# Kernel optimization log

Measured on AMD Instinct MI355X. Metric: run time of the kernel, lower is better.

The kernel has to match this reference:

```python
import jax, jax.numpy as jnp
import numpy as np

B, K, V = 8192, 1024, 2


def setup_inputs() -> dict:
    key = jax.random.key(0)
    k1, k2, k3, k4, k5, k6 = jax.random.split(key, 6)
    z = jax.random.normal(k1, (B, K), dtype=jnp.float32)
    # -1 means no intervention for that sample
    intervention_target = jax.random.randint(k2, (B,), -1, K)
    intervention_variant = jax.random.randint(k3, (B,), 0, V)
    raw_adjacency = jax.random.normal(k4, (K, K), dtype=jnp.float32) * 0.05
    intervention_means = jax.random.normal(k5, (K, V), dtype=jnp.float32)
    intervention_log_scales = jax.random.normal(k6, (K, V), dtype=jnp.float32) * 0.1
    return {
        "z": z,
        "intervention_target": intervention_target,
        "intervention_variant": intervention_variant,
        "raw_adjacency": raw_adjacency,
        "intervention_means": intervention_means,
        "intervention_log_scales": intervention_log_scales,
    }


def _scm_forward(z, target, variant, raw_adjacency, means, log_scales):
    Kd = z.shape[1]
    # strictly-lower-triangular adjacency (row j holds parents of node j)
    A = raw_adjacency * jnp.tril(jnp.ones((Kd, Kd), z.dtype), k=-1)

    def step(u, xs):
        a_row, mean_row, logsc_row, z_j, j = xs
        # forward substitution: u_j = z_j + sum_{i<j} A[j,i] * u_i
        # columns >= j of u are still zero and A row is zero there too
        value = z_j + u @ a_row  # [B]
        # intervention overwrite for samples with target == j
        m = mean_row[variant]                 # [B]
        s = jnp.exp(logsc_row[variant])       # [B]
        value = jnp.where(target == j, m + s * z_j, value)
        u = jax.lax.dynamic_update_slice(u, value[:, None], (0, j))
        return u, None

    u0 = jnp.zeros_like(z)
    xs = (A, means, log_scales, z.T, jnp.arange(Kd))
    u, _ = jax.lax.scan(step, u0, xs)
    return u


def reference(z, intervention_target, intervention_variant, raw_adjacency,
              intervention_means, intervention_log_scales):
    return _scm_forward(z, intervention_target, intervention_variant,
                        raw_adjacency, intervention_means, intervention_log_scales)
```

## Files before the change

### kernel.cpp

```cpp
#include <hip/hip_runtime.h>
#include <hip/hip_bf16.h>
#include <cstdint>

#define KDIM 1024
#define BDIM 8192
#define VDIM 2
#define NBLK 16

#if defined(__has_builtin)
#if __has_builtin(__builtin_amdgcn_global_load_lds)
#define HAS_GLL 1
#endif
#endif
#ifndef HAS_GLL
#define HAS_GLL 0
#endif

typedef __attribute__((ext_vector_type(8))) short short8;
typedef __attribute__((ext_vector_type(4))) float f32x4;

__device__ inline unsigned short f2bf(float x) {
  unsigned u = __builtin_bit_cast(unsigned, x);
  u = (u + 0x7FFFu + ((u >> 16) & 1u)) >> 16;
  return (unsigned short)u;
}

__device__ inline float bf2f(unsigned short x) {
  return __builtin_bit_cast(float, (unsigned)x << 16);
}


#define STAGE_T(DST, SRC, ROW0, COL0, LD)                                   \
  {                                                                         \
    const float* _s = (SRC);                                                \
    _Pragma("unroll") for (int _p = 0; _p < 4; ++_p) {                      \
      const int _m = _p * 16 + rw;                                          \
      float4 _v = *(const float4*)(_s + (size_t)((ROW0) + _m) * (LD) +      \
                                   (COL0) + 4 * k4);                        \
      (DST)[4 * k4 + 0][_m] = _v.x;                                         \
      (DST)[4 * k4 + 1][_m] = _v.y;                                         \
      (DST)[4 * k4 + 2][_m] = _v.z;                                         \
      (DST)[4 * k4 + 3][_m] = _v.w;                                         \
    }                                                                       \
  }

#define STAGE_D(DST, SRC, ROW0, COL0, LD)                                   \
  {                                                                         \
    const float* _s = (SRC);                                                \
    _Pragma("unroll") for (int _p = 0; _p < 4; ++_p) {                      \
      const int _kk = _p * 16 + rw;                                         \
      *(float4*)&(DST)[_kk][4 * k4] =                                       \
          *(const float4*)(_s + (size_t)((ROW0) + _kk) * (LD) + (COL0) +    \
                           4 * k4);                                         \
    }                                                                       \
  }

#define LOADR(REG, SRC, ROW0, COL0, LD)                                     \
  _Pragma("unroll") for (int _p = 0; _p < 4; ++_p) {                        \
    (REG)[_p] = *(const float4*)((SRC) +                                    \
                                 (size_t)((ROW0) + _p * 16 + rw) * (LD) +   \
                                 (COL0) + 4 * k4);                          \
  }

#define WRT_T(DST, REG)                                                     \
  _Pragma("unroll") for (int _p = 0; _p < 4; ++_p) {                        \
    const int _m = _p * 16 + rw;                                            \
    (DST)[4 * k4 + 0][_m] = (REG)[_p].x;                                    \
    (DST)[4 * k4 + 1][_m] = (REG)[_p].y;                                    \
    (DST)[4 * k4 + 2][_m] = (REG)[_p].z;                                    \
    (DST)[4 * k4 + 3][_m] = (REG)[_p].w;                                    \
  }

#define WRT_D(DST, REG)                                                     \
  _Pragma("unroll") for (int _p = 0; _p < 4; ++_p) {                        \
    *(float4*)&(DST)[_p * 16 + rw][4 * k4] = (REG)[_p];                     \
  }

#define ZERO_ACC                                                            \
  _Pragma("unroll") for (int _a = 0; _a < 4; ++_a)                          \
      _Pragma("unroll") for (int _b = 0; _b < 4; ++_b) acc[_a][_b] = 0.f;

__device__ __forceinline__ void mac64(const float (*Ls)[68],
                                      const float (*Rs)[68], int tm, int tn,
                                      float acc[4][4]) {
#pragma unroll 4
  for (int k = 0; k < 64; ++k) {
    const float4 av = *(const float4*)&Ls[k][4 * tm];
    const float4 bv = *(const float4*)&Rs[k][4 * tn];
    const float aa[4] = {av.x, av.y, av.z, av.w};
    const float bb4[4] = {bv.x, bv.y, bv.z, bv.w};
#pragma unroll
    for (int a = 0; a < 4; ++a)
#pragma unroll
      for (int b = 0; b < 4; ++b) acc[a][b] += aa[a] * bb4[b];
  }
}

#define STORE_MT(R0, C0)                                                    \
  _Pragma("unroll") for (int _a = 0; _a < 4; ++_a) {                        \
    *(float4*)(MT + (size_t)((R0) + 4 * tm + _a) * KDIM + (C0) + 4 * tn) =  \
        make_float4(acc[_a][0], acc[_a][1], acc[_a][2], acc[_a][3]);        \
  }

#define MBF_TILE(R0, C0, BUF)                                               \
  {                                                                         \
    __syncthreads();                                                        \
    _Pragma("unroll") for (int _a = 0; _a < 4; ++_a)                        \
        _Pragma("unroll") for (int _b = 0; _b < 4; ++_b)                    \
            (BUF)[4 * tm + _a][4 * tn + _b] = acc[_a][_b];                  \
    __syncthreads();                                                        \
    const int _tr = tid >> 4, _tc = tid & 15;                               \
    _Pragma("unroll") for (int _p = 0; _p < 4; ++_p) {                      \
      const int _il = _p * 16 + _tr;                                        \
      ushort4 _o;                                                           \
      _o.x = f2bf((BUF)[4 * _tc + 0][_il]);                                 \
      _o.y = f2bf((BUF)[4 * _tc + 1][_il]);                                 \
      _o.z = f2bf((BUF)[4 * _tc + 2][_il]);                                 \
      _o.w = f2bf((BUF)[4 * _tc + 3][_il]);                                 \
      *(ushort4*)(Mbf + (size_t)((C0) + _il) * KDIM + (R0) + 4 * _tc) = _o; \
    }                                                                       \
  }

__global__ __launch_bounds__(256) void comb01(const float* __restrict__ A,
                                              float* __restrict__ MT,
                                              unsigned short* __restrict__ Mbf,
                                              const float* __restrict__ Z,
                                              unsigned short* __restrict__ Zbf,
                                              int do_zbf) {
  if (blockIdx.x >= NBLK) {
    const int wid = blockIdx.x - NBLK;
    const int nw = gridDim.x - NBLK;
    const int idx0 = wid * 256 + threadIdx.x;
    const int stride = nw * 256;
    const float4 z4 = make_float4(0.f, 0.f, 0.f, 0.f);
    const uint4 u4 = make_uint4(0u, 0u, 0u, 0u);

    for (int i = idx0; i < 256 * 1024; i += stride) {
      const int blk = i >> 10, off = i & 1023;
      const int bi = blk >> 4, bj = blk & 15;
      if (bi <= bj) continue;
      *(float4*)(MT + (size_t)(bi * 64 + (off >> 4)) * KDIM + bj * 64 +
                 4 * (off & 15)) = z4;
    }
    for (int i = idx0; i < 256 * 512; i += stride) {
      const int blk = i >> 9, off = i & 511;
      const int bi = blk >> 4, bj = blk & 15;
      if (bi >= bj) continue;
      *(uint4*)(Mbf + (size_t)(bi * 64 + (off >> 3)) * KDIM + bj * 64 +
                8 * (off & 7)) = u4;
    }
    if (do_zbf) {
      for (int i = idx0; i < BDIM * KDIM / 4; i += stride) {
        float4 v = *(const float4*)(Z + 4 * (size_t)i);
        ushort4 o;
        o.x = f2bf(v.x);
        o.y = f2bf(v.y);
        o.z = f2bf(v.z);
        o.w = f2bf(v.w);
        *(ushort4*)(Zbf + 4 * (size_t)i) = o;
      }
    }
    return;
  }

  int b = blockIdx.x;
  const int rt = b & 1;
  const int jt = (b >> 1) & 1;
  const int s = b >> 2;
  const int base = s * 256;

  __shared__ float shpool[6 * 64 * 68];
  float (*Ls)[68] = (float(*)[68])(shpool);
  float (*Rs)[68] = (float(*)[68])(shpool + 4352);
  float (*tQ0L)[68] = (float(*)[68])(shpool + 2 * 4352);
  float (*tQ0H)[68] = (float(*)[68])(shpool + 3 * 4352);
  float (*tP0)[68] = (float(*)[68])(shpool + 4 * 4352);
  float (*tP1)[68] = (float(*)[68])(shpool + 5 * 4352);

  const int tid = threadIdx.x;
  const int k4 = tid & 15;
  const int rw = tid >> 4;
  const int tm = tid >> 4;
  const int tn = tid & 15;
  float acc[4][4];

  {
    float* Tt = shpool;
    float* As4 = shpool + 2 * 4352;
    const int g = tid >> 6;
    const int l = tid & 63;
    const int dbase = base + g * 64;
    float* Asg = As4 + g * 4160;

    for (int r = 0; r < 64; ++r)
      Asg[r * 65 + l] = A[(size_t)(dbase + r) * KDIM + dbase + l];
    __syncthreads();

    {
      const int h = l >> 5, c = l & 31;
      const float* Ah = Asg + (32 * h) * 65 + 32 * h;
      float m[32];
#pragma unroll
      for (int r = 0; r < 32; ++r) m[r] = (r == c) ? 1.f : 0.f;
#pragma unroll
      for (int r = 1; r < 32; ++r) {
        float a0 = 0.f, a1 = 0.f;
#pragma unroll
        for (int i = 0; i < 32; ++i) {
          if (i >= r) break;
          if (i & 1) a1 += Ah[r * 65 + i] * m[i];
          else       a0 += Ah[r * 65 + i] * m[i];
        }
        const float v = a0 + a1;
        m[r] = (r > c) ? v : m[r];
      }
      float* Th = Tt + g * 2112 + h * 1056;
#pragma unroll
      for (int r = 0; r < 32; ++r) Th[r * 33 + c] = m[r];
    }
    __syncthreads();

    const int tm8 = l >> 3, tn8 = l & 7;
    {
      float u[4][4];
#pragma unroll
      for (int a = 0; a < 4; ++a)
#pragma unroll
        for (int b2 = 0; b2 < 4; ++b2) u[a][b2] = 0.f;
      const float* T1 = Tt + g * 2112;
#pragma unroll
      for (int ki = 0; ki < 8; ++ki) {
        float4 av[4], bv[4];
#pragma unroll
        for (int a = 0; a < 4; ++a)
          av[a] = *(const float4*)&Asg[(32 + 4 * tm8 + a) * 65 + 4 * ki];
#pragma unroll
        for (int j = 0; j < 4; ++j)
          bv[j] = *(const float4*)&T1[(4 * ki + j) * 33 + 4 * tn8];
#pragma unroll
        for (int a = 0; a < 4; ++a) {
          const float aa[4] = {av[a].x, av[a].y, av[a].z, av[a].w};
#pragma unroll
          for (int j = 0; j < 4; ++j) {
            const float bb[4] = {bv[j].x, bv[j].y, bv[j].z, bv[j].w};
#pragma unroll
            for (int b2 = 0; b2 < 4; ++b2) u[a][b2] += aa[j] * bb[b2];
          }
        }
      }
#pragma unroll
      for (int a = 0; a < 4; ++a)
#pragma unroll
        for (int b2 = 0; b2 < 4; ++b2)
          Asg[(4 * tm8 + a) * 32 + 4 * tn8 + b2] = u[a][b2];
    }
    __syncthreads();

    {
      float t21[4][4];
#pragma unroll
      for (int a = 0; a < 4; ++a)
#pragma unroll
        for (int b2 = 0; b2 < 4; ++b2) t21[a][b2] = 0.f;
      const float* T2 = Tt + g * 2112 + 1056;
#pragma unroll
      for (int ki = 0; ki < 8; ++ki) {
        float4 av[4], bv[4];
#pragma unroll
        for (int a = 0; a < 4; ++a)
          av[a] = *(const float4*)&T2[(4 * tm8 + a) * 33 + 4 * ki];
#pragma unroll
        for (int j = 0; j < 4; ++j)
          bv[j] = *(const float4*)&Asg[(4 * ki + j) * 32 + 4 * tn8];
#pragma unroll
        for (int a = 0; a < 4; ++a) {
          const float aa[4] = {av[a].x, av[a].y, av[a].z, av[a].w};
#pragma unroll
          for (int j = 0; j < 4; ++j) {
            const float bb[4] = {bv[j].x, bv[j].y, bv[j].z, bv[j].w};
#pragma unroll
            for (int b2 = 0; b2 < 4; ++b2) t21[a][b2] += aa[j] * bb[b2];
          }
        }
      }
#pragma unroll
      for (int a = 0; a < 4; ++a)
#pragma unroll
        for (int b2 = 0; b2 < 4; ++b2)
          Asg[1024 + (4 * tm8 + a) * 32 + 4 * tn8 + b2] = t21[a][b2];
    }
    __syncthreads();

    {
      const float* T21 = Asg + 1024;
      const float* Tg = Tt + g * 2112;
      for (int r4 = 0; r4 < 16; ++r4) {
        float vals[4];
#pragma unroll
        for (int j = 0; j < 4; ++j) {
          const int r = 4 * r4 + j;
          float v;
          if (r < 32)
            v = (l < 32) ? Tg[r * 33 + l] : 0.f;
          else
            v = (l < 32) ? T21[(r - 32) * 32 + l]
                         : Tg[1056 + (r - 32) * 33 + (l - 32)];
          vals[j] = v;
        }
        *(float4*)(MT + (size_t)(dbase + l) * KDIM + dbase + 4 * r4) =
            make_float4(vals[0], vals[1], vals[2], vals[3]);
      }
      if (jt == 0 && rt == 0) {
        for (int r = 0; r < 64; ++r) {
          float v;
          if (r < 32)
            v = (l < 32) ? Tg[r * 33 + l] : 0.f;
          else
            v = (l < 32) ? T21[(r - 32) * 32 + l]
                         : Tg[1056 + (r - 32) * 33 + (l - 32)];
          Mbf[(size_t)(dbase + r) * KDIM + dbase + l] = f2bf(v);
        }
      }
    }
    __syncthreads();
  }

  if (jt == 0) {
    STAGE_T(Ls, MT, base, base, KDIM);
    STAGE_T(Rs, A, base + 64, base, KDIM);
    __syncthreads();
    ZERO_ACC;
    mac64(Ls, Rs, tm, tn, acc);
    __syncthreads();
#pragma unroll
    for (int a = 0; a < 4; ++a)
#pragma unroll
      for (int b2 = 0; b2 < 4; ++b2) tP0[4 * tn + b2][4 * tm + a] = acc[a][b2];
    STAGE_D(Rs, MT, base + 64, base + 64, KDIM);
    __syncthreads();
    ZERO_ACC;
    mac64(tP0, Rs, tm, tn, acc);
    __syncthreads();
#pragma unroll
    for (int a = 0; a < 4; ++a)
#pragma unroll
      for (int b2 = 0; b2 < 4; ++b2) tQ0L[4 * tn + b2][4 * tm + a] = acc[a][b2];
    if (rt == 0) {
      STORE_MT(base, base + 64);
      MBF_TILE(base, base + 64, Rs);
    }
  }
  __syncthreads();

  if (rt == 1) {
    STAGE_T(Ls, MT, base + 128, base + 128, KDIM);
    STAGE_T(Rs, A, base + 192, base + 128, KDIM);
    __syncthreads();
    ZERO_ACC;
    mac64(Ls, Rs, tm, tn, acc);
    __syncthreads();
#pragma unroll
    for (int a = 0; a < 4; ++a)
#pragma unroll
      for (int b2 = 0; b2 < 4; ++b2) tP1[4 * tn + b2][4 * tm + a] = acc[a][b2];
    STAGE_D(Rs, MT, base + 192, base + 192, KDIM);
    __syncthreads();
    ZERO_ACC;
    mac64(tP1, Rs, tm, tn, acc);
    __syncthreads();
#pragma unroll
    for (int a = 0; a < 4; ++a)
#pragma unroll
      for (int b2 = 0; b2 < 4; ++b2) tQ0H[4 * tm + a][4 * tn + b2] = acc[a][b2];
    if (jt == 1) {
      STORE_MT(base + 128, base + 192);
      MBF_TILE(base + 128, base + 192, Rs);
    }
  }
  __syncthreads();

  STAGE_T(Ls, MT, base + 64 * jt, base + 64 * jt, KDIM);
  __syncthreads();
  for (int kb2 = 0; kb2 <= rt; ++kb2) {
    ZERO_ACC;
    for (int kb = jt; kb < 2; ++kb) {
      STAGE_T(Rs, A, base + 128 + 64 * kb2, base + 64 * kb, KDIM);
      __syncthreads();
      mac64(kb == jt ? Ls : tQ0L, Rs, tm, tn, acc);
      __syncthreads();
    }
    if (kb2 == 0) {
#pragma unroll
      for (int a = 0; a < 4; ++a)
#pragma unroll
        for (int b2 = 0; b2 < 4; ++b2) tP0[4 * tn + b2][4 * tm + a] = acc[a][b2];
    } else {
#pragma unroll
      for (int a = 0; a < 4; ++a)
#pragma unroll
        for (int b2 = 0; b2 < 4; ++b2) tP1[4 * tn + b2][4 * tm + a] = acc[a][b2];
    }
  }
  __syncthreads();

  ZERO_ACC;
  if (rt == 0) {
    STAGE_D(Rs, MT, base + 128, base + 128, KDIM);
    __syncthreads();
    mac64(tP0, Rs, tm, tn, acc);
    __syncthreads();
  } else {
    mac64(tP0, tQ0H, tm, tn, acc);
    __syncthreads();
    STAGE_D(Rs, MT, base + 192, base + 192, KDIM);
    __syncthreads();
    mac64(tP1, Rs, tm, tn, acc);
    __syncthreads();
  }
  STORE_MT(base + 64 * jt, base + 128 + 64 * rt);
  MBF_TILE(base + 64 * jt, base + 128 + 64 * rt, Rs);
}

template <int T>
__global__ __launch_bounds__(256) void p_k(const float* __restrict__ A,
                                           const float* __restrict__ MT,
                                           float* __restrict__ Pt) {
  int b = blockIdx.x;
  const int rb = b % T; b /= T;
  const int jb = b % T; b /= T;
  const int c = b;
  const int h = 64 * T;
  const int base = c * 2 * h;

  __shared__ float Ls[64][68];
  __shared__ float Rs[64][68];
  const int tid = threadIdx.x;
  const int k4 = tid & 15;
  const int rw = tid >> 4;
  const int tm = tid >> 4;
  const int tn = tid & 15;
  float acc[4][4];
  ZERO_ACC;

  float4 lr[4], rr[4];
  LOADR(lr, MT, base + 64 * jb, base + 64 * jb, KDIM);
  LOADR(rr, A, base + h + 64 * rb, base + 64 * jb, KDIM);
  for (int kb = jb; kb < T; ++kb) {
    WRT_T(Ls, lr);
    WRT_T(Rs, rr);
    __syncthreads();
    if (kb + 1 < T) {
      LOADR(lr, MT, base + 64 * jb, base + 64 * (kb + 1), KDIM);
      LOADR(rr, A, base + h + 64 * rb, base + 64 * (kb + 1), KDIM);
    }
    mac64(Ls, Rs, tm, tn, acc);
    __syncthreads();
  }

  float* P0 = Pt + (size_t)c * h * h;
#pragma unroll
  for (int a = 0; a < 4; ++a)
    *(float4*)(P0 + (size_t)(64 * jb + 4 * tm + a) * h + 64 * rb + 4 * tn) =
        make_float4(acc[a][0], acc[a][1], acc[a][2], acc[a][3]);
}

template <int T>
__global__ __launch_bounds__(256) void q_k(float* __restrict__ MT,
                                           const float* __restrict__ Pt,
                                           unsigned short* __restrict__ Mbf) {
  int b = blockIdx.x;
  const int rb = b % T; b /= T;
  const int jb = b % T; b /= T;
  const int c = b;
  const int h = 64 * T;
  const int base = c * 2 * h;

  __shared__ float Ls[64][68];
  __shared__ float Rs[64][68];
  const int tid = threadIdx.x;
  const int k4 = tid & 15;
  const int rw = tid >> 4;
  const int tm = tid >> 4;
  const int tn = tid & 15;
  float acc[4][4];
  ZERO_ACC;

  const float* P0 = Pt + (size_t)c * h * h;
  float4 lr[4], rr[4];
  LOADR(lr, P0, 64 * jb, 0, h);
  LOADR(rr, MT, base + h, base + h + 64 * rb, KDIM);
  for (int kb = 0; kb <= rb; ++kb) {
    WRT_T(Ls, lr);
    WRT_D(Rs, rr);
    __syncthreads();
    if (kb + 1 <= rb) {
      LOADR(lr, P0, 64 * jb, 64 * (kb + 1), h);
      LOADR(rr, MT, base + h + 64 * (kb + 1), base + h + 64 * rb, KDIM);
    }
    mac64(Ls, Rs, tm, tn, acc);
    __syncthreads();
  }

  STORE_MT(base + 64 * jb, base + h + 64 * rb);
  MBF_TILE(base + 64 * jb, base + h + 64 * rb, Ls);
}

#define LDB 72

template <int ZBF>
__global__ __launch_bounds__(256) void gemm_mfma(
    const float* __restrict__ Z, const unsigned short* __restrict__ Zbf,
    const unsigned short* __restrict__ Mbf, const float* __restrict__ MT,
    const int* __restrict__ tgt, const int* __restrict__ var,
    const float* __restrict__ means, const float* __restrict__ lsc,
    float* __restrict__ C) {
  __shared__ unsigned short As[128][LDB];
#if HAS_GLL
  __shared__ unsigned short Bs[128][64];
#else
  __shared__ unsigned short Bs[128][LDB];
#endif
  __shared__ float scoef[128];
  __shared__ int stb[128];

  const int d = blockIdx.x;
  const int xbl = d & 7;
  const int nir = (d >> 3) & 7;
  const int xbh = d >> 6;
  const int xb = xbh * 8 + xbl;
  const int ni = (xb & 32) ? (7 - nir) : nir;
  const int b0 = xb * 128;
  const int i0 = ni * 128;

  const int tid = threadIdx.x;
  const int w = tid >> 6;
  const int lane = tid & 63;
  const int wr = w >> 1, wc = w & 1;
  const int mlane = lane & 15;
  const int q = lane >> 4;

  const int rq = tid >> 4, kq = tid & 15;
  const int cb = tid >> 3, ck = tid & 7;

  f32x4 acc[4][4];
#pragma unroll
  for (int a = 0; a < 4; ++a)
#pragma unroll
    for (int b = 0; b < 4; ++b) acc[a][b] = (f32x4){0.f, 0.f, 0.f, 0.f};

  const int nkb = 2 * (ni + 1);
  for (int kb = 0; kb < nkb; ++kb) {
    const int k0 = kb * 64;
    if (ZBF) {
#pragma unroll
      for (int p = 0; p < 4; ++p) {
        const int r = p * 32 + cb;
        *(uint4*)&As[r][8 * ck] =
            *(const uint4*)(Zbf + (size_t)(b0 + r) * KDIM + k0 + 8 * ck);
      }
    } else {
#pragma unroll
      for (int p = 0; p < 8; ++p) {
        const int r = p * 16 + rq;
        float4 zv = *(const float4*)(Z + (size_t)(b0 + r) * KDIM + k0 + 4 * kq);
        ushort4 o;
        o.x = f2bf(zv.x);
        o.y = f2bf(zv.y);
        o.z = f2bf(zv.z);
        o.w = f2bf(zv.w);
        *(ushort4*)&As[r][4 * kq] = o;
      }
    }
#if HAS_GLL
    {
      const int rl = lane >> 3;
      const int ch = lane & 7;
#pragma unroll
      for (int i = 0; i < 4; ++i) {
        const int row = w * 32 + i * 8 + rl;
        const int sch = ch ^ (row & 7);
        const unsigned short* src =
            Mbf + (size_t)(i0 + row) * KDIM + k0 + sch * 8;
        __builtin_amdgcn_global_load_lds(
            (const __attribute__((address_space(1))) void*)src,
            (__attribute__((address_space(3))) void*)&Bs[w * 32 + i * 8][0],
            16, 0, 0);
      }
    }
#else
#pragma unroll
    for (int p = 0; p < 4; ++p) {
      const int c = p * 32 + cb;
      *(uint4*)&Bs[c][8 * ck] =
          *(const uint4*)(Mbf + (size_t)(i0 + c) * KDIM + k0 + 8 * ck);
    }
#endif
    __syncthreads();
#pragma unroll
    for (int ks = 0; ks < 2; ++ks) {
      const int kf = ks * 32 + q * 8;
      short8 av[4], bv[4];
#pragma unroll
      for (int a = 0; a < 4; ++a)
        av[a] = *(const short8*)&As[wr * 64 + 16 * a + mlane][kf];
#if HAS_GLL
      const char* BsB = (const char*)&Bs[0][0];
#pragma unroll
      for (int b = 0; b < 4; ++b) {
        const int row = wc * 64 + 16 * b + mlane;
        bv[b] = *(const short8*)(BsB + row * 128 +
                                 ((2 * kf) ^ ((row & 7) << 4)));
      }
#else
#pragma unroll
      for (int b = 0; b < 4; ++b)
        bv[b] = *(const short8*)&Bs[wc * 64 + 16 * b + mlane][kf];
#endif
#pragma unroll
      for (int a = 0; a < 4; ++a)
#pragma unroll
        for (int b = 0; b < 4; ++b)
          acc[a][b] =
              __builtin_amdgcn_mfma_f32_16x16x32_bf16(av[a], bv[b], acc[a][b], 0, 0, 0);
    }
    __syncthreads();
  }

  {
    const int s = tid >> 1, h2 = tid & 1;
    const int br = b0 + s;
    const int tb = tgt[br];
    float part = 0.f;
    if (tb >= 0) {
      const int nk16 = (tb >> 4) + 1;
      if (ZBF) {
        const unsigned short* zr = Zbf + (size_t)br * KDIM;
        const unsigned short* mr = Mbf + (size_t)tb * KDIM;
        for (int c16 = h2; c16 < nk16; c16 += 2) {
          const uint4 za = *(const uint4*)(zr + c16 * 16);
          const uint4 zb2 = *(const uint4*)(zr + c16 * 16 + 8);
          const uint4 ma = *(const uint4*)(mr + c16 * 16);
          const uint4 mb2 = *(const uint4*)(mr + c16 * 16 + 8);
          const unsigned zw[8] = {za.x, za.y, za.z, za.w,
                                  zb2.x, zb2.y, zb2.z, zb2.w};
          const unsigned mw[8] = {ma.x, ma.y, ma.z, ma.w,
                                  mb2.x, mb2.y, mb2.z, mb2.w};
#pragma unroll
          for (int wv = 0; wv < 8; ++wv) {
            part += __builtin_bit_cast(float, zw[wv] << 16) *
                    __builtin_bit_cast(float, mw[wv] << 16);
            part += __builtin_bit_cast(float, zw[wv] & 0xFFFF0000u) *
                    __builtin_bit_cast(float, mw[wv] & 0xFFFF0000u);
          }
        }
      } else {
        const float* zr = Z + (size_t)br * KDIM;
        const unsigned short* mr = Mbf + (size_t)tb * KDIM;
        const int nk8 = (tb >> 3) + 1;
        for (int c8 = h2; c8 < nk8; c8 += 2) {
          const float4 z0 = *(const float4*)(zr + c8 * 8);
          const float4 z1 = *(const float4*)(zr + c8 * 8 + 4);
          const ushort4 m0 = *(const ushort4*)(mr + c8 * 8);
          const ushort4 m1 = *(const ushort4*)(mr + c8 * 8 + 4);
          part += z0.x * bf2f(m0.x) + z0.y * bf2f(m0.y) + z0.z * bf2f(m0.z) +
                  z0.w * bf2f(m0.w) + z1.x * bf2f(m1.x) + z1.y * bf2f(m1.y) +
                  z1.z * bf2f(m1.z) + z1.w * bf2f(m1.w);
        }
      }
    }
    part += __shfl_down(part, 1);
    if (h2 == 0) {
      float cf = 0.f;
      int tbs = 0;
      if (tb >= 0) {
        const int v = var[br];
        const float mval = means[tb * VDIM + v];
        const float sval = expf(lsc[tb * VDIM + v]);
        const float zv = Z[(size_t)br * KDIM + tb];
        cf = (mval + sval * zv) - part;
        tbs = tb;
      }
      scoef[s] = cf;
      stb[s] = tbs;
    }
  }
  __syncthreads();

#pragma unroll
  for (int a = 0; a < 4; ++a) {
    const int l0 = wr * 64 + 16 * a + q * 4;
    const int row0 = b0 + l0;
#pragma unroll
    for (int b = 0; b < 4; ++b) {
      const int col = i0 + wc * 64 + 16 * b + mlane;
      float* Cp = C + (size_t)row0 * KDIM + col;
#pragma unroll
      for (int j = 0; j < 4; ++j) {
        const float cf = scoef[l0 + j];
        const float corr = cf * MT[(size_t)stb[l0 + j] * KDIM + col];
        Cp[j * KDIM] = acc[a][b][j] + corr;
      }
    }
  }
}

extern "C" void kernel_launch(void* const* d_in, const int* in_sizes, int n_in,
                              void* d_out, int out_size, void* d_ws,
                              size_t ws_size, hipStream_t stream) {
  const float* z = (const float*)d_in[0];
  const int* tgt = (const int*)d_in[1];
  const int* var = (const int*)d_in[2];
  const float* A = (const float*)d_in[3];
  const float* means = (const float*)d_in[4];
  const float* lsc = (const float*)d_in[5];
  float* out = (float*)d_out;

  char* ws = (char*)d_ws;
  float* MT = (float*)ws;
  unsigned short* Mbf = (unsigned short*)(ws + (4u << 20));
  float* Pt2 = (float*)(ws + (6u << 20));
  float* Pt3 = (float*)(ws + (6u << 20) + (512u << 10));
  unsigned short* Zbf = (unsigned short*)(ws + (7u << 20) + (512u << 10));
  const int use_zbf =
      ws_size >= (7u << 20) + (512u << 10) + (size_t)BDIM * KDIM * 2 ? 1 : 0;

  hipLaunchKernelGGL(comb01, dim3(256), dim3(256), 0, stream, A, MT, Mbf, z,
                     Zbf, use_zbf);
  hipLaunchKernelGGL((p_k<4>), dim3(32), dim3(256), 0, stream, A, MT, Pt2);
  hipLaunchKernelGGL((q_k<4>), dim3(32), dim3(256), 0, stream, MT, Pt2, Mbf);
  hipLaunchKernelGGL((p_k<8>), dim3(64), dim3(256), 0, stream, A, MT, Pt3);
  hipLaunchKernelGGL((q_k<8>), dim3(64), dim3(256), 0, stream, MT, Pt3, Mbf);
  if (use_zbf)
    hipLaunchKernelGGL((gemm_mfma<1>), dim3((BDIM / 128) * (KDIM / 128)),
                       dim3(256), 0, stream, z, Zbf, Mbf, MT, tgt, var, means,
                       lsc, out);
  else
    hipLaunchKernelGGL((gemm_mfma<0>), dim3((BDIM / 128) * (KDIM / 128)),
                       dim3(256), 0, stream, z, Zbf, Mbf, MT, tgt, var, means,
                       lsc, out);
}
```

Baseline: 248.5 us.

## Split-K the triangular inverse combine steps with atomics for more parallelism

The P and Q combine kernels that build the inverse of (I - A) block by block used to loop serially over the inner 64-blocks inside each of only 32 or 64 workgroups. They are now split along the inner dimension, so each workgroup handles a single 64-block product and accumulates into P and MT with float atomics. Workgroups with no work in the triangular structure exit early. comb01 now pre-zeros the target MT tiles and the P scratch, and a new kernel converts those 96 tiles to bf16 afterwards. The aim is more parallelism on this latency-bound chain, at the cost of atomic traffic, an extra launch and an order of float summation that can vary between runs.

```diff
diff --git a/kernel.cpp b/kernel.cpp
--- a/kernel.cpp
+++ b/kernel.cpp
@@ -27,6 +27,19 @@
 
 __device__ inline float bf2f(unsigned short x) {
   return __builtin_bit_cast(float, (unsigned)x << 16);
+}
+
+__device__ inline void qtile_map(int t, int& bi, int& bj) {
+  if (t < 64) {
+    bi = t >> 3;
+    bj = 8 + (t & 7);
+  } else {
+    int r = t - 64;
+    const int c = r >> 4;
+    r &= 15;
+    bi = 8 * c + (r >> 2);
+    bj = 8 * c + 4 + (r & 3);
+  }
 }
 
 
@@ -53,27 +66,6 @@
           *(const float4*)(_s + (size_t)((ROW0) + _kk) * (LD) + (COL0) +    \
                            4 * k4);                                         \
     }                                                                       \
-  }
-
-#define LOADR(REG, SRC, ROW0, COL0, LD)                                     \
-  _Pragma("unroll") for (int _p = 0; _p < 4; ++_p) {                        \
-    (REG)[_p] = *(const float4*)((SRC) +                                    \
-                                 (size_t)((ROW0) + _p * 16 + rw) * (LD) +   \
-                                 (COL0) + 4 * k4);                          \
-  }
-
-#define WRT_T(DST, REG)                                                     \
-  _Pragma("unroll") for (int _p = 0; _p < 4; ++_p) {                        \
-    const int _m = _p * 16 + rw;                                            \
-    (DST)[4 * k4 + 0][_m] = (REG)[_p].x;                                    \
-    (DST)[4 * k4 + 1][_m] = (REG)[_p].y;                                    \
-    (DST)[4 * k4 + 2][_m] = (REG)[_p].z;                                    \
-    (DST)[4 * k4 + 3][_m] = (REG)[_p].w;                                    \
-  }
-
-#define WRT_D(DST, REG)                                                     \
-  _Pragma("unroll") for (int _p = 0; _p < 4; ++_p) {                        \
-    *(float4*)&(DST)[_p * 16 + rw][4 * k4] = (REG)[_p];                     \
   }
 
 #define ZERO_ACC                                                            \
@@ -126,6 +118,7 @@
                                               unsigned short* __restrict__ Mbf,
                                               const float* __restrict__ Z,
                                               unsigned short* __restrict__ Zbf,
+                                              float* __restrict__ Pscr,
                                               int do_zbf) {
   if (blockIdx.x >= NBLK) {
     const int wid = blockIdx.x - NBLK;
@@ -142,6 +135,15 @@
       *(float4*)(MT + (size_t)(bi * 64 + (off >> 4)) * KDIM + bj * 64 +
                  4 * (off & 15)) = z4;
     }
+    for (int i = idx0; i < 96 * 1024; i += stride) {
+      const int t = i >> 10, off = i & 1023;
+      int bi, bj;
+      qtile_map(t, bi, bj);
+      *(float4*)(MT + (size_t)(bi * 64 + (off >> 4)) * KDIM + bj * 64 +
+                 4 * (off & 15)) = z4;
+    }
+    for (int i = idx0; i < 98304; i += stride)
+      *(float4*)(Pscr + 4 * (size_t)i) = z4;
     for (int i = idx0; i < 256 * 512; i += stride) {
       const int blk = i >> 9, off = i & 511;
       const int bi = blk >> 4, bj = blk & 15;
@@ -422,13 +424,15 @@
 }
 
 template <int T>
-__global__ __launch_bounds__(256) void p_k(const float* __restrict__ A,
-                                           const float* __restrict__ MT,
-                                           float* __restrict__ Pt) {
+__global__ __launch_bounds__(256) void comb_p(const float* __restrict__ A,
+                                              const float* __restrict__ MT,
+                                              float* __restrict__ Pt) {
   int b = blockIdx.x;
-  const int rb = b % T; b /= T;
-  const int jb = b % T; b /= T;
+  const int kc = b % T; b /= T;
+  const int rt = b % T; b /= T;
+  const int jt = b % T; b /= T;
   const int c = b;
+  if (kc < jt) return;
   const int h = 64 * T;
   const int base = c * 2 * h;
 
@@ -442,36 +446,30 @@
   float acc[4][4];
   ZERO_ACC;
 
-  float4 lr[4], rr[4];
-  LOADR(lr, MT, base + 64 * jb, base + 64 * jb, KDIM);
-  LOADR(rr, A, base + h + 64 * rb, base + 64 * jb, KDIM);
-  for (int kb = jb; kb < T; ++kb) {
-    WRT_T(Ls, lr);
-    WRT_T(Rs, rr);
-    __syncthreads();
-    if (kb + 1 < T) {
-      LOADR(lr, MT, base + 64 * jb, base + 64 * (kb + 1), KDIM);
-      LOADR(rr, A, base + h + 64 * rb, base + 64 * (kb + 1), KDIM);
-    }
-    mac64(Ls, Rs, tm, tn, acc);
-    __syncthreads();
-  }
+  STAGE_T(Ls, MT, base + 64 * jt, base + 64 * kc, KDIM);
+  STAGE_T(Rs, A, base + h + 64 * rt, base + 64 * kc, KDIM);
+  __syncthreads();
+  mac64(Ls, Rs, tm, tn, acc);
 
   float* P0 = Pt + (size_t)c * h * h;
 #pragma unroll
   for (int a = 0; a < 4; ++a)
-    *(float4*)(P0 + (size_t)(64 * jb + 4 * tm + a) * h + 64 * rb + 4 * tn) =
-        make_float4(acc[a][0], acc[a][1], acc[a][2], acc[a][3]);
+#pragma unroll
+    for (int b2 = 0; b2 < 4; ++b2)
+      unsafeAtomicAdd(P0 + (size_t)(64 * jt + 4 * tm + a) * h + 64 * rt +
+                          4 * tn + b2,
+                      acc[a][b2]);
 }
 
 template <int T>
-__global__ __launch_bounds__(256) void q_k(float* __restrict__ MT,
-                                           const float* __restrict__ Pt,
-                                           unsigned short* __restrict__ Mbf) {
+__global__ __launch_bounds__(256) void comb_q(float* __restrict__ MT,
+                                              const float* __restrict__ Pt) {
   int b = blockIdx.x;
-  const int rb = b % T; b /= T;
-  const int jb = b % T; b /= T;
+  const int kc = b % T; b /= T;
+  const int rt = b % T; b /= T;
+  const int jt = b % T; b /= T;
   const int c = b;
+  if (kc > rt) return;
   const int h = 64 * T;
   const int base = c * 2 * h;
 
@@ -486,23 +484,50 @@
   ZERO_ACC;
 
   const float* P0 = Pt + (size_t)c * h * h;
-  float4 lr[4], rr[4];
-  LOADR(lr, P0, 64 * jb, 0, h);
-  LOADR(rr, MT, base + h, base + h + 64 * rb, KDIM);
-  for (int kb = 0; kb <= rb; ++kb) {
-    WRT_T(Ls, lr);
-    WRT_D(Rs, rr);
-    __syncthreads();
-    if (kb + 1 <= rb) {
-      LOADR(lr, P0, 64 * jb, 64 * (kb + 1), h);
-      LOADR(rr, MT, base + h + 64 * (kb + 1), base + h + 64 * rb, KDIM);
-    }
-    mac64(Ls, Rs, tm, tn, acc);
-    __syncthreads();
-  }
-
-  STORE_MT(base + 64 * jb, base + h + 64 * rb);
-  MBF_TILE(base + 64 * jb, base + h + 64 * rb, Ls);
+  STAGE_T(Ls, P0, 64 * jt, 64 * kc, h);
+  STAGE_D(Rs, MT, base + h + 64 * kc, base + h + 64 * rt, KDIM);
+  __syncthreads();
+  mac64(Ls, Rs, tm, tn, acc);
+
+#pragma unroll
+  for (int a = 0; a < 4; ++a)
+#pragma unroll
+    for (int b2 = 0; b2 < 4; ++b2)
+      unsafeAtomicAdd(MT + (size_t)(base + 64 * jt + 4 * tm + a) * KDIM +
+                          base + h + 64 * rt + 4 * tn + b2,
+                      acc[a][b2]);
+}
+
+__global__ __launch_bounds__(256) void mt2bf96(const float* __restrict__ MT,
+                                               unsigned short* __restrict__ Mbf) {
+  int bi, bj;
+  qtile_map(blockIdx.x, bi, bj);
+  const int j0 = bi * 64;
+  const int i0 = bj * 64;
+  __shared__ float tile[64][65];
+
+  const int tr = threadIdx.x >> 4;
+  const int tc = threadIdx.x & 15;
+#pragma unroll
+  for (int p = 0; p < 4; ++p) {
+    const int rj = p * 16 + tr;
+    float4 v = *(const float4*)(MT + (size_t)(j0 + rj) * KDIM + i0 + 4 * tc);
+    tile[rj][4 * tc + 0] = v.x;
+    tile[rj][4 * tc + 1] = v.y;
+    tile[rj][4 * tc + 2] = v.z;
+    tile[rj][4 * tc + 3] = v.w;
+  }
+  __syncthreads();
+#pragma unroll
+  for (int p = 0; p < 4; ++p) {
+    const int il = p * 16 + tr;
+    ushort4 o;
+    o.x = f2bf(tile[4 * tc + 0][il]);
+    o.y = f2bf(tile[4 * tc + 1][il]);
+    o.z = f2bf(tile[4 * tc + 2][il]);
+    o.w = f2bf(tile[4 * tc + 3][il]);
+    *(ushort4*)(Mbf + (size_t)(i0 + il) * KDIM + j0 + 4 * tc) = o;
+  }
 }
 
 #define LDB 72
@@ -725,11 +750,12 @@
       ws_size >= (7u << 20) + (512u << 10) + (size_t)BDIM * KDIM * 2 ? 1 : 0;
 
   hipLaunchKernelGGL(comb01, dim3(256), dim3(256), 0, stream, A, MT, Mbf, z,
-                     Zbf, use_zbf);
-  hipLaunchKernelGGL((p_k<4>), dim3(32), dim3(256), 0, stream, A, MT, Pt2);
-  hipLaunchKernelGGL((q_k<4>), dim3(32), dim3(256), 0, stream, MT, Pt2, Mbf);
-  hipLaunchKernelGGL((p_k<8>), dim3(64), dim3(256), 0, stream, A, MT, Pt3);
-  hipLaunchKernelGGL((q_k<8>), dim3(64), dim3(256), 0, stream, MT, Pt3, Mbf);
+                     Zbf, Pt2, use_zbf);
+  hipLaunchKernelGGL((comb_p<4>), dim3(128), dim3(256), 0, stream, A, MT, Pt2);
+  hipLaunchKernelGGL((comb_q<4>), dim3(128), dim3(256), 0, stream, MT, Pt2);
+  hipLaunchKernelGGL((comb_p<8>), dim3(512), dim3(256), 0, stream, A, MT, Pt3);
+  hipLaunchKernelGGL((comb_q<8>), dim3(512), dim3(256), 0, stream, MT, Pt3);
+  hipLaunchKernelGGL(mt2bf96, dim3(96), dim3(256), 0, stream, MT, Mbf);
   if (use_zbf)
     hipLaunchKernelGGL((gemm_mfma<1>), dim3((BDIM / 128) * (KDIM / 128)),
                        dim3(256), 0, stream, z, Zbf, Mbf, MT, tgt, var, means,
```

Measured after the change: 228.7 us. 1.09x faster.
